# Kernel optimization log

Measured on AMD Instinct MI355X. Metric: run time of the kernel, lower is better.

Reference implementation:

```python
import jax, jax.numpy as jnp
import numpy as np

DIM = 256; D_STATE = 16; D_CONV = 4; EXPAND = 2; NS = 64
D_INNER = EXPAND * DIM; DT_RANK = (DIM + 15) // 16
B_SZ = 2; H = 64; W = 64


def setup_inputs() -> dict:
    key = jax.random.key(0)
    ks = jax.random.split(key, 32)
    g = lambda i, shape, s=0.02: jax.random.normal(ks[i], shape, dtype=jnp.float32) * s
    inp = {}
    inp["x"] = jax.random.normal(ks[0], (B_SZ, DIM, H, W), dtype=jnp.float32)
    inp["ln_w"] = jnp.ones((DIM,), jnp.float32)
    inp["ln_b"] = jnp.zeros((DIM,), jnp.float32)
    inp["in_proj_w"] = g(1, (2 * D_INNER, DIM))
    for suf, base in (("", 2), ("_b", 10), ("_s", 18)):
        inp["conv_w" + suf] = g(base, (D_INNER, D_CONV), 0.1)
        inp["conv_b" + suf] = g(base + 1, (D_INNER,), 0.1)
        inp["x_proj_w" + suf] = g(base + 2, (DT_RANK + 2 * D_STATE, D_INNER))
        inp["dt_proj_w" + suf] = g(base + 3, (D_INNER, DT_RANK), 0.1)
        inp["dt_proj_b" + suf] = g(base + 4, (D_INNER,), 0.5)
        inp["D" + suf] = jnp.ones((D_INNER,), jnp.float32)
    A_log = jnp.tile(jnp.log(jnp.arange(1, D_STATE + 1, dtype=jnp.float32)), (D_INNER, 1))
    inp["A_log"] = A_log
    inp["A_log_b"] = A_log
    inp["A_log_s"] = A_log
    inp["out_proj_w"] = g(26, (DIM, D_INNER))
    return inp


def _silu(x):
    return x * jax.nn.sigmoid(x)


def _causal_conv(x, w, b):
    # x: (B, L, D); w: (D, K) depthwise causal conv along L
    K = w.shape[1]; L = x.shape[1]
    xp = jnp.pad(x, ((0, 0), (K - 1, 0), (0, 0)))
    y = b
    for k in range(K):
        y = y + xp[:, k:k + L, :] * w[:, k]
    return y


def _ssm_dir(x, z, conv_w, conv_b, x_proj_w, dt_proj_w, dt_proj_b, A_log, Dp):
    # one directional Mamba inner fn (no out_proj); x, z: (B, L, d_inner)
    Bsz, L, Din = x.shape
    xc = _silu(_causal_conv(x, conv_w, conv_b))
    x_dbl = xc @ x_proj_w.T  # (B, L, dt_rank + 2*d_state)
    dt_r = x_dbl[..., :DT_RANK]
    Bm = x_dbl[..., DT_RANK:DT_RANK + D_STATE]
    Cm = x_dbl[..., DT_RANK + D_STATE:]
    dt = jax.nn.softplus(dt_r @ dt_proj_w.T + dt_proj_b)  # (B, L, d_inner)
    A = -jnp.exp(A_log)  # (d_inner, d_state)

    def step(h, inp):
        dt_t, x_t, B_t, C_t = inp
        dA = jnp.exp(dt_t[..., None] * A)  # (B, d_inner, d_state)
        h = dA * h + (dt_t * x_t)[..., None] * B_t[:, None, :]
        return h, jnp.einsum('bds,bs->bd', h, C_t)

    h0 = jnp.zeros((Bsz, Din, D_STATE), x.dtype)
    _, ys = jax.lax.scan(step, h0, (dt.transpose(1, 0, 2), xc.transpose(1, 0, 2),
                                    Bm.transpose(1, 0, 2), Cm.transpose(1, 0, 2)))
    y = ys.transpose(1, 0, 2) + xc * Dp
    return y * _silu(z)


def reference(x, ln_w, ln_b, in_proj_w,
              conv_w, conv_b, x_proj_w, dt_proj_w, dt_proj_b, D,
              conv_w_b, conv_b_b, x_proj_w_b, dt_proj_w_b, dt_proj_b_b, D_b,
              conv_w_s, conv_b_s, x_proj_w_s, dt_proj_w_s, dt_proj_b_s, D_s,
              A_log, A_log_b, A_log_s, out_proj_w):
    Bsz, C, Hh, Ww = x.shape
    L = Hh * Ww
    xf = x.reshape(Bsz, C, L).transpose(0, 2, 1)  # (B, L, C)
    mu = xf.mean(-1, keepdims=True)
    var = ((xf - mu) ** 2).mean(-1, keepdims=True)
    xn = (xf - mu) / jnp.sqrt(var + 1e-5) * ln_w + ln_b
    xz = xn @ in_proj_w.T  # (B, L, 2*d_inner), shared across directions
    xin, z = xz[..., :D_INNER], xz[..., D_INNER:]
    # forward scan
    y_f = _ssm_dir(xin, z, conv_w, conv_b, x_proj_w, dt_proj_w, dt_proj_b, A_log, D)
    # backward scan (flip sequence, scan, flip back)
    y_b = _ssm_dir(xin[:, ::-1], z[:, ::-1], conv_w_b, conv_b_b, x_proj_w_b,
                   dt_proj_w_b, dt_proj_b_b, A_log_b, D_b)[:, ::-1]
    # slice-interleaved scan: 'b (s i) d -> b (i s) d' with s = NS slices
    def il(t):
        return t.reshape(Bsz, NS, L // NS, D_INNER).transpose(0, 2, 1, 3).reshape(Bsz, L, D_INNER)
    def dil(t):
        return t.reshape(Bsz, L // NS, NS, D_INNER).transpose(0, 2, 1, 3).reshape(Bsz, L, D_INNER)
    y_s = dil(_ssm_dir(il(xin), il(z), conv_w_s, conv_b_s, x_proj_w_s,
                       dt_proj_w_s, dt_proj_b_s, A_log_s, D_s))
    out = (y_f + y_b + y_s) @ out_proj_w.T  # (B, L, C)
    return x + out.transpose(0, 2, 1).reshape(Bsz, C, Hh, Ww)
```

## Files before the change

### kernel.cpp

```cpp
#include <hip/hip_runtime.h>
#include <hip/hip_bf16.h>
#include <cstdint>

#define B_SZ 2
#define DIM 256
#define L_SEQ 4096
#define D_INNER 512
#define DT_RANK 16
#define D_STATE 16
#define NCHUNK 128
#define CHUNK 32

static constexpr size_t SZ_BIG_SH = (size_t)B_SZ * L_SEQ * D_INNER;

typedef __attribute__((ext_vector_type(8))) short short8v;
typedef __attribute__((ext_vector_type(4))) short short4v;
typedef __attribute__((ext_vector_type(4))) float f32x4;

__device__ __forceinline__ float silu_f(float v) {
    return v / (1.0f + __expf(-v));
}
__device__ __forceinline__ float softplus_fast(float v) {
    return (v > 15.0f) ? v : __logf(1.0f + __expf(v));
}
__device__ __forceinline__ short f2bf(float f) {
    uint32_t u = __float_as_uint(f);
    u += 0x7fffu + ((u >> 16) & 1u);
    return (short)(u >> 16);
}
__device__ __forceinline__ float bf2f(short s) {
    return __uint_as_float(((uint32_t)(uint16_t)s) << 16);
}
__device__ __forceinline__ int dir_map(int p, int dm) {
    if (dm == 0) return p;
    if (dm == 1) return (L_SEQ - 1) - p;
    return ((p & 63) << 6) | (p >> 6);
}
__device__ __forceinline__ void pow_dA(float r1, float* dA) {
    const float r2 = r1 * r1, r4 = r2 * r2, r8 = r4 * r4;
    dA[0] = r1;         dA[1] = r2;         dA[2] = r2 * r1;    dA[3] = r4;
    dA[4] = r4 * r1;    dA[5] = r4 * r2;    dA[6] = r4 * dA[2]; dA[7] = r8;
    dA[8] = r8 * r1;    dA[9] = r8 * r2;    dA[10] = r8 * dA[2]; dA[11] = r8 * r4;
    dA[12] = r8 * dA[4]; dA[13] = r8 * dA[5]; dA[14] = r8 * dA[6]; dA[15] = r8 * r8;
}

__global__ __launch_bounds__(256) void k_cvt(
    const float* __restrict__ Wi, const float* __restrict__ Wo,
    const float* __restrict__ xp0, const float* __restrict__ xp1, const float* __restrict__ xp2,
    const float* __restrict__ dw0, const float* __restrict__ dw1, const float* __restrict__ dw2,
    short* __restrict__ Wib, short* __restrict__ Wob,
    short* __restrict__ xpwb, short* __restrict__ dtwb)
{
    const int idx = blockIdx.x * 256 + threadIdx.x;
    const float* src; short* dst; int off;
    if (idx < 65536)        { src = Wi; dst = Wib; off = idx; }
    else if (idx < 98304)   { src = Wo; dst = Wob; off = idx - 65536; }
    else if (idx < 116736)  {
        int k = idx - 98304; const int d = k / 6144; k -= d * 6144;
        src = d == 0 ? xp0 : (d == 1 ? xp1 : xp2);
        dst = xpwb + (size_t)d * 24576; off = k;
    } else {
        int k = idx - 116736; const int d = k / 2048; k -= d * 2048;
        src = d == 0 ? dw0 : (d == 1 ? dw1 : dw2);
        dst = dtwb + (size_t)d * 8192; off = k;
    }
    const float4 v = *(const float4*)(src + (size_t)off * 4);
    short4v p = {f2bf(v.x), f2bf(v.y), f2bf(v.z), f2bf(v.w)};
    *(short4v*)(dst + (size_t)off * 4) = p;
}

__global__ __launch_bounds__(256) void k_ln_t(
    const float* __restrict__ x, const float* __restrict__ lnw,
    const float* __restrict__ lnb, short* __restrict__ xnb)
{
    __shared__ float xt[64][257];
    __shared__ float red[2][4][64];
    __shared__ float muS[64], rsS[64];
    __shared__ float lnwS[DIM], lnbS[DIM];

    const int b  = blockIdx.x >> 6;
    const int l0 = (blockIdx.x & 63) << 6;
    const int t  = threadIdx.x;
    lnwS[t] = lnw[t]; lnbS[t] = lnb[t];

    const float* xb = x + (size_t)b * DIM * L_SEQ + l0;
#pragma unroll
    for (int it = 0; it < 16; ++it) {
        const int idx = it * 256 + t;
        const int c = idx >> 4, pos = (idx & 15) << 2;
        const float4 v = *(const float4*)(xb + (size_t)c * L_SEQ + pos);
        xt[pos + 0][c] = v.x; xt[pos + 1][c] = v.y;
        xt[pos + 2][c] = v.z; xt[pos + 3][c] = v.w;
    }
    __syncthreads();
    {
        const int l = t & 63, cq = t >> 6;
        float sum = 0.f, sq = 0.f;
        for (int c = cq * 64; c < cq * 64 + 64; ++c) {
            const float v = xt[l][c];
            sum += v; sq += v * v;
        }
        red[0][cq][l] = sum; red[1][cq][l] = sq;
    }
    __syncthreads();
    if (t < 64) {
        const float s  = red[0][0][t] + red[0][1][t] + red[0][2][t] + red[0][3][t];
        const float q2 = red[1][0][t] + red[1][1][t] + red[1][2][t] + red[1][3][t];
        const float mu  = s * (1.0f / DIM);
        const float var = q2 * (1.0f / DIM) - mu * mu;
        muS[t] = mu; rsS[t] = rsqrtf(var + 1e-5f);
    }
    __syncthreads();
#pragma unroll
    for (int it = 0; it < 32; ++it) {
        const int idx = it * 256 + t;
        const int l = idx >> 7, cp = (idx & 127) << 1;
        const float mu = muS[l], rs = rsS[l];
        short2 p;
        p.x = f2bf((xt[l][cp + 0] - mu) * rs * lnwS[cp + 0] + lnbS[cp + 0]);
        p.y = f2bf((xt[l][cp + 1] - mu) * rs * lnwS[cp + 1] + lnbS[cp + 1]);
        *(short2*)(xnb + (size_t)((b * L_SEQ) + l0 + l) * DIM + cp) = p;
    }
}

__global__ __launch_bounds__(256) void k_inproj_mfma(
    const short* __restrict__ xnb, const short* __restrict__ Wib,
    short* __restrict__ xinb, short* __restrict__ szb)
{
    const int mblk = blockIdx.x >> 2;
    const int q    = blockIdx.x & 3;
    const int t = threadIdx.x;
    const int w = t >> 6, l = t & 63;
    const int m0 = mblk * 64 + w * 16;
    const int n0 = q * 256;
    const int lrow = l & 15, lk = l >> 4;

    short8v a[8];
    {
        const short* ap = xnb + (size_t)(m0 + lrow) * DIM + lk * 8;
#pragma unroll
        for (int kk = 0; kk < 8; ++kk)
            a[kk] = *(const short8v*)(ap + kk * 32);
    }

#pragma unroll 4
    for (int nf = 0; nf < 16; ++nf) {
        const int n = n0 + nf * 16 + lrow;
        const short* bp = Wib + (size_t)n * DIM + lk * 8;
        f32x4 acc = {0.f, 0.f, 0.f, 0.f};
#pragma unroll
        for (int kk = 0; kk < 8; ++kk)
            acc = __builtin_amdgcn_mfma_f32_16x16x32_bf16(
                a[kk], *(const short8v*)(bp + kk * 32), acc, 0, 0, 0);
        const int col = n;
        const int r0  = m0 + lk * 4;
        if (n0 < D_INNER) {
#pragma unroll
            for (int j = 0; j < 4; ++j)
                xinb[(size_t)(r0 + j) * D_INNER + col] = f2bf(acc[j]);
        } else {
#pragma unroll
            for (int j = 0; j < 4; ++j)
                szb[(size_t)(r0 + j) * D_INNER + (col - D_INNER)] = f2bf(silu_f(acc[j]));
        }
    }
}

__global__ __launch_bounds__(256) void k_conv3(
    const short* __restrict__ xinb,
    const float* __restrict__ cw0, const float* __restrict__ cw1, const float* __restrict__ cw2,
    const float* __restrict__ cb0, const float* __restrict__ cb1, const float* __restrict__ cb2,
    short* __restrict__ xcbb, int dir_base, size_t xcb_str)
{
    const int rel = blockIdx.x >> 9;
    const int rem = blockIdx.x & 511;
    const int dir = dir_base + rel;
    const int b   = rem >> 8;
    const int p0  = (rem & 255) << 4;
    const int t   = threadIdx.x;

    const float* cw = dir == 0 ? cw0 : (dir == 1 ? cw1 : cw2);
    const float* cb = dir == 0 ? cb0 : (dir == 1 ? cb1 : cb2);
    short* xcb = xcbb + (size_t)rel * xcb_str;

    __shared__ short s[19][D_INNER];
    for (int i = 0; i < 19; ++i) {
        const int pk = p0 - 3 + i;
        short2 v = {0, 0};
        if (pk >= 0) {
            const int lo = dir_map(pk, dir);
            v = *(const short2*)(xinb + ((size_t)b * L_SEQ + lo) * D_INNER + t * 2);
        }
        *(short2*)&s[i][t * 2] = v;
    }
    __syncthreads();

#pragma unroll
    for (int half = 0; half < 2; ++half) {
        const int d = half * 256 + t;
        const float4 wv = *(const float4*)(cw + d * 4);
        const float bb = cb[d];
        float x0 = bf2f(s[0][d]), x1 = bf2f(s[1][d]), x2 = bf2f(s[2][d]);
#pragma unroll
        for (int i = 0; i < 16; ++i) {
            const float x3 = bf2f(s[i + 3][d]);
            const float a = bb + wv.x * x0 + wv.y * x1 + wv.z * x2 + wv.w * x3;
            xcb[((size_t)b * L_SEQ + p0 + i) * D_INNER + d] = f2bf(silu_f(a));
            x0 = x1; x1 = x2; x2 = x3;
        }
    }
}

__global__ __launch_bounds__(256) void k_proj3_mfma(
    const short* __restrict__ xcbb, const short* __restrict__ xpwb,
    const short* __restrict__ dtwb,
    const float* __restrict__ dtb0, const float* __restrict__ dtb1, const float* __restrict__ dtb2,
    short* __restrict__ dtYb, float* __restrict__ bcbuf,
    int dir_base, size_t xcb_str, size_t bc_str)
{
    const int rel = blockIdx.x >> 9;
    const int rem = blockIdx.x & 511;
    const int dir = dir_base + rel;
    const int m0  = rem * 16;
    const int t = threadIdx.x;
    const int w = t >> 6, l = t & 63;
    const int lrow = l & 15, lk = l >> 4;

    const short* xcb = xcbb + (size_t)rel * xcb_str;
    const short* xpw = xpwb + (size_t)dir * (48 * 512);
    const short* dtw = dtwb + (size_t)dir * (512 * 16);
    const float* dtb = dir == 0 ? dtb0 : (dir == 1 ? dtb1 : dtb2);
    short* dt = dtYb + (size_t)dir * SZ_BIG_SH;
    float* bc = bcbuf + (size_t)rel * bc_str;

    __shared__ float red[4][3][16][17];
    __shared__ short xdblb[16][16];
    __shared__ float dtbS[512];

    dtbS[t] = dtb[t]; dtbS[t + 256] = dtb[t + 256];

    short8v a[4];
    {
        const short* ap = xcb + (size_t)(m0 + lrow) * D_INNER + w * 128 + lk * 8;
#pragma unroll
        for (int kk = 0; kk < 4; ++kk)
            a[kk] = *(const short8v*)(ap + kk * 32);
    }

#pragma unroll
    for (int nf = 0; nf < 3; ++nf) {
        f32x4 acc = {0.f, 0.f, 0.f, 0.f};
        const short* bp = xpw + (size_t)(nf * 16 + lrow) * D_INNER + w * 128 + lk * 8;
#pragma unroll
        for (int kk = 0; kk < 4; ++kk)
            acc = __builtin_amdgcn_mfma_f32_16x16x32_bf16(
                a[kk], *(const short8v*)(bp + kk * 32), acc, 0, 0, 0);
#pragma unroll
        for (int j = 0; j < 4; ++j)
            red[w][nf][lk * 4 + j][lrow] = acc[j];
    }
    __syncthreads();

#pragma unroll
    for (int i = 0; i < 3; ++i) {
        const int nf = i;
        const int row = (t >> 4) & 15, col = t & 15;
        const float v = red[0][nf][row][col] + red[1][nf][row][col]
                      + red[2][nf][row][col] + red[3][nf][row][col];
        if (nf == 0) xdblb[row][col] = f2bf(v);
        else         bc[(size_t)(m0 + row) * 32 + (nf - 1) * 16 + col] = v;
    }
    __syncthreads();

    short8v adt = {0, 0, 0, 0, 0, 0, 0, 0};
    if (lk < 2) adt = *(const short8v*)&xdblb[lrow][lk * 8];

#pragma unroll
    for (int nbw = 0; nbw < 8; ++nbw) {
        const int nb = w * 8 + nbw;
        short8v bdt = {0, 0, 0, 0, 0, 0, 0, 0};
        if (lk < 2) bdt = *(const short8v*)(dtw + (size_t)(nb * 16 + lrow) * 16 + lk * 8);
        f32x4 acc = {0.f, 0.f, 0.f, 0.f};
        acc = __builtin_amdgcn_mfma_f32_16x16x32_bf16(adt, bdt, acc, 0, 0, 0);
        const int d = nb * 16 + lrow;
        const float bias = dtbS[d];
#pragma unroll
        for (int j = 0; j < 4; ++j)
            dt[(size_t)(m0 + lk * 4 + j) * D_INNER + d] = f2bf(softplus_fast(acc[j] + bias));
    }
}

template<bool FAST>
__device__ __forceinline__ void scan1_body(
    const short* dtp, const short* xcp, const float* bcp,
    short (*dts)[256], short (*xcs)[256], float (*bcs)[16],
    const float* Al_d, int t, float* Pb_o, float* Fb_o)
{
    float As20, As2[16];
    if (FAST) {
        As20 = -__expf(Al_d[0]) * 1.44269504f;
    } else {
#pragma unroll
        for (int s = 0; s < 16; ++s) As2[s] = -__expf(Al_d[s]) * 1.44269504f;
        As20 = As2[0];
    }
    float h[16];
#pragma unroll
    for (int s = 0; s < 16; ++s) h[s] = 0.f;
    float sumdt = 0.f;

    for (int tile = 0; tile < CHUNK / 16; ++tile) {
        const int p0 = tile * 16;
#pragma unroll
        for (int rep = 0; rep < 2; ++rep) {
            const int idx = rep * 256 + t;
            const int jr = idx >> 5, c8 = (idx & 31) << 3;
            *(short8v*)&dts[jr][c8] = *(const short8v*)(dtp + (size_t)(p0 + jr) * D_INNER + c8);
            *(short8v*)&xcs[jr][c8] = *(const short8v*)(xcp + (size_t)(p0 + jr) * D_INNER + c8);
        }
        if (t < 64) {
            const int jr = t >> 2, c4 = (t & 3) << 2;
            *(float4*)&bcs[jr][c4] = *(const float4*)(bcp + (size_t)(p0 + jr) * 32 + c4);
        }
        __syncthreads();

#pragma unroll
        for (int j = 0; j < 16; ++j) {
            const float dtv = bf2f(dts[j][t]);
            const float xv  = bf2f(xcs[j][t]);
            sumdt += dtv;
            const float dtx = dtv * xv;
            float Bv[16];
#pragma unroll
            for (int s4 = 0; s4 < 4; ++s4) {
                const float4 bb = *(const float4*)&bcs[j][s4 * 4];
                Bv[s4 * 4 + 0] = bb.x; Bv[s4 * 4 + 1] = bb.y;
                Bv[s4 * 4 + 2] = bb.z; Bv[s4 * 4 + 3] = bb.w;
            }
            if (FAST) {
                float dA[16];
                pow_dA(exp2f(dtv * As20), dA);
#pragma unroll
                for (int s = 0; s < 16; ++s)
                    h[s] = fmaf(dA[s], h[s], dtx * Bv[s]);
            } else {
#pragma unroll
                for (int s = 0; s < 16; ++s)
                    h[s] = fmaf(exp2f(dtv * As2[s]), h[s], dtx * Bv[s]);
            }
        }
        __syncthreads();
    }
    if (FAST) {
        float Pv[16];
        pow_dA(exp2f(sumdt * As20), Pv);
#pragma unroll
        for (int s = 0; s < 16; ++s) {
            Pb_o[s] = Pv[s];
            Fb_o[s] = h[s];
        }
    } else {
#pragma unroll
        for (int s = 0; s < 16; ++s) {
            Pb_o[s] = exp2f(As2[s] * sumdt);
            Fb_o[s] = h[s];
        }
    }
}

template<bool FAST>
__device__ __forceinline__ void scan2_body(
    short* dtp, const short* xcp, const float* bcp,
    short (*dts)[256], short (*xcs)[256], float (*bcs)[32],
    const float* Al_d, int t, float Dv, const float* Hin_o)
{
    float As20, As2[16];
    if (FAST) {
        As20 = -__expf(Al_d[0]) * 1.44269504f;
    } else {
#pragma unroll
        for (int s = 0; s < 16; ++s) As2[s] = -__expf(Al_d[s]) * 1.44269504f;
        As20 = As2[0];
    }
    float h[16];
#pragma unroll
    for (int s4 = 0; s4 < 4; ++s4) {
        const float4 hv = *(const float4*)(Hin_o + s4 * 4);
        h[s4 * 4 + 0] = hv.x; h[s4 * 4 + 1] = hv.y;
        h[s4 * 4 + 2] = hv.z; h[s4 * 4 + 3] = hv.w;
    }

    for (int tile = 0; tile < CHUNK / 16; ++tile) {
        const int p0 = tile * 16;
#pragma unroll
        for (int rep = 0; rep < 2; ++rep) {
            const int idx = rep * 256 + t;
            const int jr = idx >> 5, c8 = (idx & 31) << 3;
            *(short8v*)&dts[jr][c8] = *(const short8v*)(dtp + (size_t)(p0 + jr) * D_INNER + c8);
            *(short8v*)&xcs[jr][c8] = *(const short8v*)(xcp + (size_t)(p0 + jr) * D_INNER + c8);
        }
        if (t < 128) {
            const int jr = t >> 3, c4 = (t & 7) << 2;
            *(float4*)&bcs[jr][c4] = *(const float4*)(bcp + (size_t)(p0 + jr) * 32 + c4);
        }
        __syncthreads();

#pragma unroll
        for (int j = 0; j < 16; ++j) {
            const float dtv = bf2f(dts[j][t]);
            const float xv  = bf2f(xcs[j][t]);
            const float dtx = dtv * xv;
            float Bv[16], Cv[16];
#pragma unroll
            for (int s4 = 0; s4 < 4; ++s4) {
                const float4 bb = *(const float4*)&bcs[j][s4 * 4];
                const float4 cc = *(const float4*)&bcs[j][16 + s4 * 4];
                Bv[s4 * 4 + 0] = bb.x; Bv[s4 * 4 + 1] = bb.y;
                Bv[s4 * 4 + 2] = bb.z; Bv[s4 * 4 + 3] = bb.w;
                Cv[s4 * 4 + 0] = cc.x; Cv[s4 * 4 + 1] = cc.y;
                Cv[s4 * 4 + 2] = cc.z; Cv[s4 * 4 + 3] = cc.w;
            }
            float y = xv * Dv;
            if (FAST) {
                float dA[16];
                pow_dA(exp2f(dtv * As20), dA);
#pragma unroll
                for (int s = 0; s < 16; ++s) {
                    h[s] = fmaf(dA[s], h[s], dtx * Bv[s]);
                    y = fmaf(h[s], Cv[s], y);
                }
            } else {
#pragma unroll
                for (int s = 0; s < 16; ++s) {
                    h[s] = fmaf(exp2f(dtv * As2[s]), h[s], dtx * Bv[s]);
                    y = fmaf(h[s], Cv[s], y);
                }
            }
            dtp[(size_t)(p0 + j) * D_INNER + t] = f2bf(y);
        }
        __syncthreads();
    }
}

__device__ __forceinline__ bool fast_vote(const float* Al_d, int t, int* flagS) {
    bool ok = true;
    const float a0 = __expf(Al_d[0]);
#pragma unroll
    for (int s = 1; s < 16; ++s) {
        const float v = __expf(Al_d[s]);
        const float e = (float)(s + 1) * a0;
        ok = ok && (fabsf(v - e) <= 1e-3f * e);
    }
    if (t == 0) *flagS = 1;
    __syncthreads();
    if (!ok) *flagS = 0;
    __syncthreads();
    return *flagS != 0;
}

__global__ __launch_bounds__(256, 4) void k_scan1(
    const short* __restrict__ dtYb, const short* __restrict__ xcbb,
    const float* __restrict__ bcb,
    const float* __restrict__ Al0, const float* __restrict__ Al1, const float* __restrict__ Al2,
    float* __restrict__ Pbb, float* __restrict__ Fbb,
    int dir_base, size_t xcb_str, size_t bc_str, size_t pf_str)
{
    const int rel = blockIdx.x >> 9;
    const int rem = blockIdx.x & 511;
    const int dir = dir_base + rel;
    const int b     = rem >> 8;
    const int chunk = (rem >> 1) & 127;
    const int half  = rem & 1;
    const int t = threadIdx.x;
    const int d = half * 256 + t;

    const short* dtg = dtYb + (size_t)dir * SZ_BIG_SH;
    const short* xcg = xcbb + (size_t)rel * xcb_str;
    const float* bcg = bcb + (size_t)rel * bc_str;
    const float* Al = dir == 0 ? Al0 : (dir == 1 ? Al1 : Al2);
    float* Pb = Pbb + (size_t)rel * pf_str;
    float* Fb = Fbb + (size_t)rel * pf_str;

    __shared__ short dts[16][256];
    __shared__ short xcs[16][256];
    __shared__ float bcs[16][16];
    __shared__ int flagS;

    const size_t rowbase = (size_t)b * L_SEQ + chunk * CHUNK;
    const short* dtp = dtg + rowbase * D_INNER + half * 256;
    const short* xcp = xcg + rowbase * D_INNER + half * 256;
    const float* bcp = bcg + rowbase * 32;
    const float* Al_d = Al + d * D_STATE;
    const size_t o = (((size_t)b * NCHUNK + chunk) * D_INNER + d) * D_STATE;

    const bool fast = fast_vote(Al_d, t, &flagS);
    if (fast) scan1_body<true >(dtp, xcp, bcp, dts, xcs, bcs, Al_d, t, Pb + o, Fb + o);
    else      scan1_body<false>(dtp, xcp, bcp, dts, xcs, bcs, Al_d, t, Pb + o, Fb + o);
}

__global__ __launch_bounds__(256) void k_comb(
    float* __restrict__ PbHin, const float* __restrict__ Fbb, size_t pf_str)
{
    const int rel = blockIdx.x >> 6;
    const int gid = (blockIdx.x & 63) * 256 + threadIdx.x;
    const int b   = gid >> 13;
    const int rem = gid & 8191;
    float* PH = PbHin + (size_t)rel * pf_str;
    const float* Fb = Fbb + (size_t)rel * pf_str;
    float h = 0.f;
    for (int c = 0; c < NCHUNK; ++c) {
        const size_t i = ((size_t)(b * NCHUNK + c) << 13) + rem;
        const float pv = PH[i];
        const float fv = Fb[i];
        PH[i] = h;
        h = fv + pv * h;
    }
}

__global__ __launch_bounds__(256, 4) void k_scan2(
    short* dtYb,
    const short* __restrict__ xcbb, const float* __restrict__ bcb,
    const float* __restrict__ Al0, const float* __restrict__ Al1, const float* __restrict__ Al2,
    const float* __restrict__ Dp0, const float* __restrict__ Dp1, const float* __restrict__ Dp2,
    const float* __restrict__ Hinb,
    int dir_base, size_t xcb_str, size_t bc_str, size_t pf_str)
{
    const int rel = blockIdx.x >> 9;
    const int rem = blockIdx.x & 511;
    const int dir = dir_base + rel;
    const int b     = rem >> 8;
    const int chunk = (rem >> 1) & 127;
    const int half  = rem & 1;
    const int t = threadIdx.x;
    const int d = half * 256 + t;

    short* dtg      = dtYb + (size_t)dir * SZ_BIG_SH;
    const short* xcg = xcbb + (size_t)rel * xcb_str;
    const float* bcg = bcb + (size_t)rel * bc_str;
    const float* Al  = dir == 0 ? Al0 : (dir == 1 ? Al1 : Al2);
    const float* Dpp = dir == 0 ? Dp0 : (dir == 1 ? Dp1 : Dp2);
    const float* Hin = Hinb + (size_t)rel * pf_str;

    __shared__ short dts[16][256];
    __shared__ short xcs[16][256];
    __shared__ float bcs[16][32];
    __shared__ int flagS;

    const size_t rowbase = (size_t)b * L_SEQ + chunk * CHUNK;
    short* dtp       = dtg + rowbase * D_INNER + half * 256;
    const short* xcp = xcg + rowbase * D_INNER + half * 256;
    const float* bcp = bcg + rowbase * 32;
    const float* Al_d = Al + d * D_STATE;
    const float Dv = Dpp[d];
    const size_t o = (((size_t)b * NCHUNK + chunk) * D_INNER + d) * D_STATE;

    const bool fast = fast_vote(Al_d, t, &flagS);
    if (fast) scan2_body<true >(dtp, xcp, bcp, dts, xcs, bcs, Al_d, t, Dv, Hin + o);
    else      scan2_body<false>(dtp, xcp, bcp, dts, xcs, bcs, Al_d, t, Dv, Hin + o);
}

__global__ __launch_bounds__(256) void k_out3_mfma(
    const short* __restrict__ yall, const short* __restrict__ szb,
    const short* __restrict__ Wob, const float* __restrict__ x,
    float* __restrict__ out)
{
    __shared__ short ytb[32][512];
    const int tile = blockIdx.x;
    const int b  = tile >> 7;
    const int l0 = (tile & 127) << 5;
    const int t  = threadIdx.x;

    const short* y0 = yall;
    const short* y1 = yall + SZ_BIG_SH;
    const short* y2 = yall + 2 * SZ_BIG_SH;
    const size_t rb = (size_t)b * L_SEQ;

#pragma unroll
    for (int it = 0; it < 8; ++it) {
        const int idx = it * 256 + t;
        const int r  = idx >> 6;
        const int c8 = idx & 63;
        const int lrow = l0 + r;
        const int p1 = (L_SEQ - 1) - lrow;
        const int p2 = ((lrow & 63) << 6) | (lrow >> 6);
        const short8v s0 = *(const short8v*)(y0 + (rb + lrow) * D_INNER + c8 * 8);
        const short8v s1 = *(const short8v*)(y1 + (rb + p1)   * D_INNER + c8 * 8);
        const short8v s2 = *(const short8v*)(y2 + (rb + p2)   * D_INNER + c8 * 8);
        const short8v sv = *(const short8v*)(szb + (rb + lrow) * D_INNER + c8 * 8);
        short8v pk;
#pragma unroll
        for (int i = 0; i < 8; ++i)
            pk[i] = f2bf((bf2f(s0[i]) + bf2f(s1[i]) + bf2f(s2[i])) * bf2f(sv[i]));
        *(short8v*)&ytb[r][(c8 ^ (r & 7)) * 8] = pk;
    }
    __syncthreads();

    const int w = t >> 6, l = t & 63;
    const int lrow = l & 15, lk = l >> 4;
    const int nf = w & 1;
    const int j0 = (w >> 1) * 128;
    const int brow = nf * 16 + lrow;

    f32x4 acc[8];
#pragma unroll
    for (int jf = 0; jf < 8; ++jf) acc[jf] = {0.f, 0.f, 0.f, 0.f};

#pragma unroll 4
    for (int kk = 0; kk < 16; ++kk) {
        const int c8 = kk * 4 + lk;
        const short8v bfrag = *(const short8v*)&ytb[brow][(c8 ^ (brow & 7)) * 8];
#pragma unroll
        for (int jf = 0; jf < 8; ++jf) {
            const short8v afrag = *(const short8v*)(
                Wob + (size_t)(j0 + jf * 16 + lrow) * D_INNER + kk * 32 + lk * 8);
            acc[jf] = __builtin_amdgcn_mfma_f32_16x16x32_bf16(afrag, bfrag, acc[jf], 0, 0, 0);
        }
    }

    const int lcol = l0 + nf * 16 + lrow;
#pragma unroll
    for (int jf = 0; jf < 8; ++jf) {
        const int jr0 = j0 + jf * 16 + lk * 4;
#pragma unroll
        for (int j = 0; j < 4; ++j) {
            const size_t o = ((size_t)b * DIM + jr0 + j) * L_SEQ + lcol;
            out[o] = x[o] + acc[jf][j];
        }
    }
}

extern "C" void kernel_launch(void* const* d_in, const int* in_sizes, int n_in,
                              void* d_out, int out_size, void* d_ws, size_t ws_size,
                              hipStream_t stream)
{
    const float* x       = (const float*)d_in[0];
    const float* ln_w    = (const float*)d_in[1];
    const float* ln_b    = (const float*)d_in[2];
    const float* in_proj = (const float*)d_in[3];
    const float* conv_w[3] = {(const float*)d_in[4],  (const float*)d_in[10], (const float*)d_in[16]};
    const float* conv_b[3] = {(const float*)d_in[5],  (const float*)d_in[11], (const float*)d_in[17]};
    const float* xpw[3]    = {(const float*)d_in[6],  (const float*)d_in[12], (const float*)d_in[18]};
    const float* dtw[3]    = {(const float*)d_in[7],  (const float*)d_in[13], (const float*)d_in[19]};
    const float* dtb[3]    = {(const float*)d_in[8],  (const float*)d_in[14], (const float*)d_in[20]};
    const float* Dp[3]     = {(const float*)d_in[9],  (const float*)d_in[15], (const float*)d_in[21]};
    const float* A_log[3]  = {(const float*)d_in[22], (const float*)d_in[23], (const float*)d_in[24]};
    const float* out_proj  = (const float*)d_in[25];
    float* out = (float*)d_out;
    (void)in_sizes; (void)n_in; (void)out_size;

    const size_t NROW   = (size_t)B_SZ * L_SEQ;
    const size_t SZ_XNB = NROW * DIM / 2;
    const size_t SZ_WIB = 262144 / 2;
    const size_t SZ_WOB = 131072 / 2;
    const size_t SZ_XPW = 3 * 24576 / 2;
    const size_t SZ_DTW = 3 * 8192 / 2;
    const size_t SZ_BH  = NROW * D_INNER / 2;
    const size_t SZ_BC  = NROW * 32;
    const size_t SZ_PF  = (size_t)B_SZ * NCHUNK * D_INNER * D_STATE;

    const size_t need_merged =
        SZ_XNB + SZ_WIB + SZ_WOB + SZ_XPW + SZ_DTW +
        2 * SZ_BH + 3 * SZ_BH + 3 * SZ_BH + 3 * SZ_BC + 6 * SZ_PF;
    const bool merged = ws_size >= need_merged * sizeof(float);
    const int ndir = merged ? 3 : 1;
    const size_t xcb_str = merged ? (SZ_BH * 2) : 0;
    const size_t bc_str  = merged ? SZ_BC : 0;
    const size_t pf_str  = merged ? SZ_PF : 0;

    float* ws   = (float*)d_ws;
    float* p    = ws;
    short* xnb  = (short*)p;  p += SZ_XNB;
    short* Wib  = (short*)p;  p += SZ_WIB;
    short* Wob  = (short*)p;  p += SZ_WOB;
    short* xpwb = (short*)p;  p += SZ_XPW;
    short* dtwb = (short*)p;  p += SZ_DTW;
    short* xinb = (short*)p;  p += SZ_BH;
    short* szb  = (short*)p;  p += SZ_BH;
    short* dtYb = (short*)p;  p += 3 * SZ_BH;
    short* xcbb = (short*)p;  p += (size_t)ndir * SZ_BH;
    float* bc   = p;          p += (size_t)ndir * SZ_BC;
    float* Pb   = p;          p += (size_t)ndir * SZ_PF;
    float* Fb   = p;          p += (size_t)ndir * SZ_PF;

    k_cvt<<<dim3(480), dim3(256), 0, stream>>>(
        in_proj, out_proj, xpw[0], xpw[1], xpw[2], dtw[0], dtw[1], dtw[2],
        Wib, Wob, xpwb, dtwb);
    k_ln_t<<<dim3(B_SZ * 64), dim3(256), 0, stream>>>(x, ln_w, ln_b, xnb);
    k_inproj_mfma<<<dim3(512), dim3(256), 0, stream>>>(xnb, Wib, xinb, szb);

    for (int d0 = 0; d0 < 3; d0 += ndir) {
        k_conv3<<<dim3(512 * ndir), dim3(256), 0, stream>>>(
            xinb, conv_w[0], conv_w[1], conv_w[2],
            conv_b[0], conv_b[1], conv_b[2], xcbb, d0, xcb_str);
        k_proj3_mfma<<<dim3(512 * ndir), dim3(256), 0, stream>>>(
            xcbb, xpwb, dtwb, dtb[0], dtb[1], dtb[2],
            dtYb, bc, d0, xcb_str, bc_str);
        k_scan1<<<dim3(512 * ndir), dim3(256), 0, stream>>>(
            dtYb, xcbb, bc, A_log[0], A_log[1], A_log[2], Pb, Fb,
            d0, xcb_str, bc_str, pf_str);
        k_comb<<<dim3(64 * ndir), dim3(256), 0, stream>>>(Pb, Fb, pf_str);
        k_scan2<<<dim3(512 * ndir), dim3(256), 0, stream>>>(
            dtYb, xcbb, bc, A_log[0], A_log[1], A_log[2],
            Dp[0], Dp[1], Dp[2], Pb, d0, xcb_str, bc_str, pf_str);
    }

    k_out3_mfma<<<dim3(256), dim3(256), 0, stream>>>(
        dtYb, szb, Wob, x, out);
}
```

Measured before the change: 265.9 us.

## Store chunk sum of dt instead of decay products and transpose carry layout

Scan pass 1 now writes only the chunk's accumulated dt (one float per channel) rather than 16 per-state decay factors. The combine kernel recomputes each decay as exp2(A*sumdt). The carry-state buffer layout changes from [chunk][d][s] to [chunk][s][d], so per-thread writes in scan1 and reads in scan2 are strided by D_INNER, while the combine kernel's reads over d stay contiguous. This roughly halves the intermediate traffic and workspace for the chunked scan, at the cost of one extra exp per element in the combine step.

```diff
diff --git a/kernel.cpp b/kernel.cpp
--- a/kernel.cpp
+++ b/kernel.cpp
@@ -12,6 +12,8 @@
 #define CHUNK 32
 
 static constexpr size_t SZ_BIG_SH = (size_t)B_SZ * L_SEQ * D_INNER;
+static constexpr size_t F_DIR  = (size_t)B_SZ * NCHUNK * D_STATE * D_INNER;
+static constexpr size_t SD_DIR = (size_t)B_SZ * NCHUNK * D_INNER;
 
 typedef __attribute__((ext_vector_type(8))) short short8v;
 typedef __attribute__((ext_vector_type(4))) short short4v;
@@ -290,11 +292,27 @@
     }
 }
 
+__device__ __forceinline__ bool fast_vote(const float* Al_d, int t, int* flagS) {
+    bool ok = true;
+    const float a0 = __expf(Al_d[0]);
+#pragma unroll
+    for (int s = 1; s < 16; ++s) {
+        const float v = __expf(Al_d[s]);
+        const float e = (float)(s + 1) * a0;
+        ok = ok && (fabsf(v - e) <= 1e-3f * e);
+    }
+    if (t == 0) *flagS = 1;
+    __syncthreads();
+    if (!ok) *flagS = 0;
+    __syncthreads();
+    return *flagS != 0;
+}
+
 template<bool FAST>
 __device__ __forceinline__ void scan1_body(
     const short* dtp, const short* xcp, const float* bcp,
     short (*dts)[256], short (*xcs)[256], float (*bcs)[16],
-    const float* Al_d, int t, float* Pb_o, float* Fb_o)
+    const float* Al_d, int t, float* F_o, float* SD_o)
 {
     float As20, As2[16];
     if (FAST) {
@@ -351,21 +369,10 @@
         }
         __syncthreads();
     }
-    if (FAST) {
-        float Pv[16];
-        pow_dA(exp2f(sumdt * As20), Pv);
-#pragma unroll
-        for (int s = 0; s < 16; ++s) {
-            Pb_o[s] = Pv[s];
-            Fb_o[s] = h[s];
-        }
-    } else {
-#pragma unroll
-        for (int s = 0; s < 16; ++s) {
-            Pb_o[s] = exp2f(As2[s] * sumdt);
-            Fb_o[s] = h[s];
-        }
-    }
+#pragma unroll
+    for (int s = 0; s < 16; ++s)
+        F_o[(size_t)s * D_INNER] = h[s];
+    *SD_o = sumdt;
 }
 
 template<bool FAST>
@@ -384,11 +391,8 @@
     }
     float h[16];
 #pragma unroll
-    for (int s4 = 0; s4 < 4; ++s4) {
-        const float4 hv = *(const float4*)(Hin_o + s4 * 4);
-        h[s4 * 4 + 0] = hv.x; h[s4 * 4 + 1] = hv.y;
-        h[s4 * 4 + 2] = hv.z; h[s4 * 4 + 3] = hv.w;
-    }
+    for (int s = 0; s < 16; ++s)
+        h[s] = Hin_o[(size_t)s * D_INNER];
 
     for (int tile = 0; tile < CHUNK / 16; ++tile) {
         const int p0 = tile * 16;
@@ -442,28 +446,12 @@
     }
 }
 
-__device__ __forceinline__ bool fast_vote(const float* Al_d, int t, int* flagS) {
-    bool ok = true;
-    const float a0 = __expf(Al_d[0]);
-#pragma unroll
-    for (int s = 1; s < 16; ++s) {
-        const float v = __expf(Al_d[s]);
-        const float e = (float)(s + 1) * a0;
-        ok = ok && (fabsf(v - e) <= 1e-3f * e);
-    }
-    if (t == 0) *flagS = 1;
-    __syncthreads();
-    if (!ok) *flagS = 0;
-    __syncthreads();
-    return *flagS != 0;
-}
-
 __global__ __launch_bounds__(256, 4) void k_scan1(
     const short* __restrict__ dtYb, const short* __restrict__ xcbb,
     const float* __restrict__ bcb,
     const float* __restrict__ Al0, const float* __restrict__ Al1, const float* __restrict__ Al2,
-    float* __restrict__ Pbb, float* __restrict__ Fbb,
-    int dir_base, size_t xcb_str, size_t bc_str, size_t pf_str)
+    float* __restrict__ Fg, float* __restrict__ SDg,
+    int dir_base, size_t xcb_str, size_t bc_str)
 {
     const int rel = blockIdx.x >> 9;
     const int rem = blockIdx.x & 511;
@@ -478,8 +466,8 @@
     const short* xcg = xcbb + (size_t)rel * xcb_str;
     const float* bcg = bcb + (size_t)rel * bc_str;
     const float* Al = dir == 0 ? Al0 : (dir == 1 ? Al1 : Al2);
-    float* Pb = Pbb + (size_t)rel * pf_str;
-    float* Fb = Fbb + (size_t)rel * pf_str;
+    float* F  = Fg  + (size_t)rel * F_DIR;
+    float* SD = SDg + (size_t)rel * SD_DIR;
 
     __shared__ short dts[16][256];
     __shared__ short xcs[16][256];
@@ -491,29 +479,42 @@
     const short* xcp = xcg + rowbase * D_INNER + half * 256;
     const float* bcp = bcg + rowbase * 32;
     const float* Al_d = Al + d * D_STATE;
-    const size_t o = (((size_t)b * NCHUNK + chunk) * D_INNER + d) * D_STATE;
+    const size_t fo  = ((size_t)b * NCHUNK + chunk) * (D_STATE * D_INNER) + d;
+    const size_t sdo = ((size_t)b * NCHUNK + chunk) * D_INNER + d;
 
     const bool fast = fast_vote(Al_d, t, &flagS);
-    if (fast) scan1_body<true >(dtp, xcp, bcp, dts, xcs, bcs, Al_d, t, Pb + o, Fb + o);
-    else      scan1_body<false>(dtp, xcp, bcp, dts, xcs, bcs, Al_d, t, Pb + o, Fb + o);
+    if (fast) scan1_body<true >(dtp, xcp, bcp, dts, xcs, bcs, Al_d, t, F + fo, SD + sdo);
+    else      scan1_body<false>(dtp, xcp, bcp, dts, xcs, bcs, Al_d, t, F + fo, SD + sdo);
 }
 
 __global__ __launch_bounds__(256) void k_comb(
-    float* __restrict__ PbHin, const float* __restrict__ Fbb, size_t pf_str)
+    float* __restrict__ Fg, const float* __restrict__ SDg,
+    const float* __restrict__ Al0, const float* __restrict__ Al1, const float* __restrict__ Al2,
+    int dir_base)
 {
     const int rel = blockIdx.x >> 6;
+    const int dir = dir_base + rel;
     const int gid = (blockIdx.x & 63) * 256 + threadIdx.x;
     const int b   = gid >> 13;
     const int rem = gid & 8191;
-    float* PH = PbHin + (size_t)rel * pf_str;
-    const float* Fb = Fbb + (size_t)rel * pf_str;
+    const int s   = rem >> 9;
+    const int d   = rem & 511;
+
+    const float* Al = dir == 0 ? Al0 : (dir == 1 ? Al1 : Al2);
+    const float As2 = -__expf(Al[d * D_STATE + s]) * 1.44269504f;
+
+    float* F        = Fg  + (size_t)rel * F_DIR;
+    const float* SD = SDg + (size_t)rel * SD_DIR;
+
     float h = 0.f;
     for (int c = 0; c < NCHUNK; ++c) {
-        const size_t i = ((size_t)(b * NCHUNK + c) << 13) + rem;
-        const float pv = PH[i];
-        const float fv = Fb[i];
-        PH[i] = h;
-        h = fv + pv * h;
+        const size_t base = (size_t)(b * NCHUNK + c);
+        const size_t i  = (base << 13) + rem;
+        const float sd  = SD[(base << 9) + d];
+        const float P   = exp2f(As2 * sd);
+        const float fv  = F[i];
+        F[i] = h;
+        h = fmaf(P, h, fv);
     }
 }
 
@@ -522,8 +523,8 @@
     const short* __restrict__ xcbb, const float* __restrict__ bcb,
     const float* __restrict__ Al0, const float* __restrict__ Al1, const float* __restrict__ Al2,
     const float* __restrict__ Dp0, const float* __restrict__ Dp1, const float* __restrict__ Dp2,
-    const float* __restrict__ Hinb,
-    int dir_base, size_t xcb_str, size_t bc_str, size_t pf_str)
+    const float* __restrict__ Hing,
+    int dir_base, size_t xcb_str, size_t bc_str)
 {
     const int rel = blockIdx.x >> 9;
     const int rem = blockIdx.x & 511;
@@ -539,7 +540,7 @@
     const float* bcg = bcb + (size_t)rel * bc_str;
     const float* Al  = dir == 0 ? Al0 : (dir == 1 ? Al1 : Al2);
     const float* Dpp = dir == 0 ? Dp0 : (dir == 1 ? Dp1 : Dp2);
-    const float* Hin = Hinb + (size_t)rel * pf_str;
+    const float* Hin = Hing + (size_t)rel * F_DIR;
 
     __shared__ short dts[16][256];
     __shared__ short xcs[16][256];
@@ -552,11 +553,11 @@
     const float* bcp = bcg + rowbase * 32;
     const float* Al_d = Al + d * D_STATE;
     const float Dv = Dpp[d];
-    const size_t o = (((size_t)b * NCHUNK + chunk) * D_INNER + d) * D_STATE;
+    const size_t fo = ((size_t)b * NCHUNK + chunk) * (D_STATE * D_INNER) + d;
 
     const bool fast = fast_vote(Al_d, t, &flagS);
-    if (fast) scan2_body<true >(dtp, xcp, bcp, dts, xcs, bcs, Al_d, t, Dv, Hin + o);
-    else      scan2_body<false>(dtp, xcp, bcp, dts, xcs, bcs, Al_d, t, Dv, Hin + o);
+    if (fast) scan2_body<true >(dtp, xcp, bcp, dts, xcs, bcs, Al_d, t, Dv, Hin + fo);
+    else      scan2_body<false>(dtp, xcp, bcp, dts, xcs, bcs, Al_d, t, Dv, Hin + fo);
 }
 
 __global__ __launch_bounds__(256) void k_out3_mfma(
@@ -656,16 +657,14 @@
     const size_t SZ_DTW = 3 * 8192 / 2;
     const size_t SZ_BH  = NROW * D_INNER / 2;
     const size_t SZ_BC  = NROW * 32;
-    const size_t SZ_PF  = (size_t)B_SZ * NCHUNK * D_INNER * D_STATE;
 
     const size_t need_merged =
         SZ_XNB + SZ_WIB + SZ_WOB + SZ_XPW + SZ_DTW +
-        2 * SZ_BH + 3 * SZ_BH + 3 * SZ_BH + 3 * SZ_BC + 6 * SZ_PF;
+        2 * SZ_BH + 3 * SZ_BH + 3 * SZ_BH + 3 * SZ_BC + 3 * (F_DIR + SD_DIR);
     const bool merged = ws_size >= need_merged * sizeof(float);
     const int ndir = merged ? 3 : 1;
     const size_t xcb_str = merged ? (SZ_BH * 2) : 0;
     const size_t bc_str  = merged ? SZ_BC : 0;
-    const size_t pf_str  = merged ? SZ_PF : 0;
 
     float* ws   = (float*)d_ws;
     float* p    = ws;
@@ -679,8 +678,8 @@
     short* dtYb = (short*)p;  p += 3 * SZ_BH;
     short* xcbb = (short*)p;  p += (size_t)ndir * SZ_BH;
     float* bc   = p;          p += (size_t)ndir * SZ_BC;
-    float* Pb   = p;          p += (size_t)ndir * SZ_PF;
-    float* Fb   = p;          p += (size_t)ndir * SZ_PF;
+    float* Fg   = p;          p += (size_t)ndir * F_DIR;
+    float* SDg  = p;          p += (size_t)ndir * SD_DIR;
 
     k_cvt<<<dim3(480), dim3(256), 0, stream>>>(
         in_proj, out_proj, xpw[0], xpw[1], xpw[2], dtw[0], dtw[1], dtw[2],
@@ -696,12 +695,13 @@
             xcbb, xpwb, dtwb, dtb[0], dtb[1], dtb[2],
             dtYb, bc, d0, xcb_str, bc_str);
         k_scan1<<<dim3(512 * ndir), dim3(256), 0, stream>>>(
-            dtYb, xcbb, bc, A_log[0], A_log[1], A_log[2], Pb, Fb,
-            d0, xcb_str, bc_str, pf_str);
-        k_comb<<<dim3(64 * ndir), dim3(256), 0, stream>>>(Pb, Fb, pf_str);
+            dtYb, xcbb, bc, A_log[0], A_log[1], A_log[2], Fg, SDg,
+            d0, xcb_str, bc_str);
+        k_comb<<<dim3(64 * ndir), dim3(256), 0, stream>>>(
+            Fg, SDg, A_log[0], A_log[1], A_log[2], d0);
         k_scan2<<<dim3(512 * ndir), dim3(256), 0, stream>>>(
             dtYb, xcbb, bc, A_log[0], A_log[1], A_log[2],
-            Dp[0], Dp[1], Dp[2], Pb, d0, xcb_str, bc_str, pf_str);
+            Dp[0], Dp[1], Dp[2], Fg, d0, xcb_str, bc_str);
     }
 
     k_out3_mfma<<<dim3(256), dim3(256), 0, stream>>>(
```

Result: faster. 235.8 us (-11.3%).
